# Kernel optimization log

Hardware: AMD Instinct MI355X
Metric: run time of the kernel (lower is better)

The kernel has to match this reference:

```python
import jax, jax.numpy as jnp
import numpy as np


def setup_inputs() -> dict:
    key = jax.random.key(0)
    k1, k2, k3, k4 = jax.random.split(key, 4)
    B, C, H, W = 8, 256, 64, 64
    x = jax.random.normal(k1, (B, C, H, W), dtype=jnp.float32)
    wq = jax.random.normal(k2, (1, C), dtype=jnp.float32) * (1.0 / np.sqrt(C))
    wk = jax.random.normal(k3, (1, C), dtype=jnp.float32) * (1.0 / np.sqrt(C))
    wv = jax.random.normal(k4, (C, C), dtype=jnp.float32) * (1.0 / np.sqrt(C))
    gamma = jnp.zeros((1,), dtype=jnp.float32)
    return {"x": x, "wq": wq, "wk": wk, "wv": wv, "gamma": gamma}


def reference(x, wq, wk, wv, gamma):
    B, C, H, W = x.shape
    N = H * W
    xf = x.reshape(B, C, N)                      # [B, C, N]
    # 1x1 convs == channel matmuls
    f = jnp.einsum('oc,bcn->bon', wq, xf)        # [B, 1, N]
    g = jnp.einsum('oc,bcn->bon', wk, xf)        # [B, 1, N]
    h = jnp.einsum('oc,bcn->bon', wv, xf)        # [B, C, N]
    # scores[b, i, j] = f[b, 0, i] * g[b, 0, j]  -> [B, N, N]
    scores = jnp.einsum('bi,bj->bij', f[:, 0, :], g[:, 0, :])
    # softmax over dim=1 (rows), matching torch F.softmax(..., dim=1)
    beta = jax.nn.softmax(scores, axis=1)        # [B, N, N]
    gam = gamma[0]
    o = (1.0 - gam) * jnp.einsum('bcn,bnm->bcm', h, beta) + gam * xf
    return o.reshape(B, C, H, W)
```

## Files before the change

### kernel.cpp

```cpp
#include <hip/hip_runtime.h>
#include <math.h>

#define BQ 8
#define CQ 256
#define NQ 4096
#define MT 128
#define NSUP 64

typedef short s16x8 __attribute__((ext_vector_type(8)));
typedef short s16x4 __attribute__((ext_vector_type(4)));
typedef float f32x4 __attribute__((ext_vector_type(4)));
typedef float f32x16 __attribute__((ext_vector_type(16)));
typedef unsigned int uint;

static __device__ __forceinline__ float4 ld4(const float* p) { return *(const float4*)p; }

static constexpr float LOG2E = 1.4426950408889634f;

static __device__ __forceinline__ short f2bf(float f) {
    return __builtin_bit_cast(short, (__bf16)f);
}
static __device__ __forceinline__ uint fkey(float f) {
    uint b = __builtin_bit_cast(uint, f);
    return b ^ (0x80000000u | (uint)((int)b >> 31));
}
static __device__ __forceinline__ float fdec(uint u) {
    uint b = (u & 0x80000000u) ? (u ^ 0x80000000u) : ~u;
    return __builtin_bit_cast(float, b);
}

__global__ void k_fg(const float* __restrict__ x, const float* __restrict__ wq,
                     const float* __restrict__ wk, float* __restrict__ fs,
                     float* __restrict__ g, short* __restrict__ xbf,
                     uint* __restrict__ fmxu, uint* __restrict__ fmnu) {
    int b = blockIdx.y;
    int t = threadIdx.x;
    int nl = (t & 31) * 2;
    int cg = t >> 5;
    int n = blockIdx.x * 64 + nl;
    const float* xb = x + (size_t)b * CQ * NQ + n;
    uint* xo = (uint*)(xbf + (size_t)b * CQ * NQ + n);
    float f0 = 0.f, f1 = 0.f, g0 = 0.f, g1 = 0.f;
    int c0 = cg * 32;
#pragma unroll 8
    for (int c = c0; c < c0 + 32; ++c) {
        float2 v = *(const float2*)&xb[(size_t)c * NQ];
        f0 = fmaf(wq[c], v.x, f0);
        f1 = fmaf(wq[c], v.y, f1);
        g0 = fmaf(wk[c], v.x, g0);
        g1 = fmaf(wk[c], v.y, g1);
        uint p = (uint)(unsigned short)f2bf(v.x) | ((uint)(unsigned short)f2bf(v.y) << 16);
        xo[c * (NQ / 2)] = p;
    }
    __shared__ float sf[8][64], sg2[8][64];
    sf[cg][nl] = f0;  sf[cg][nl + 1] = f1;
    sg2[cg][nl] = g0; sg2[cg][nl + 1] = g1;
    __syncthreads();
    if (t < 64) {
        float f = 0.f, gg = 0.f;
#pragma unroll
        for (int i = 0; i < 8; ++i) { f += sf[i][t]; gg += sg2[i][t]; }
        f *= LOG2E;
        fs[b * NQ + blockIdx.x * 64 + t] = f;
        g[b * NQ + blockIdx.x * 64 + t]  = gg;
        float mx = f, mn = f;
#pragma unroll
        for (int off = 32; off; off >>= 1) {
            mx = fmaxf(mx, __shfl_xor(mx, off));
            mn = fminf(mn, __shfl_xor(mn, off));
        }
        if (t == 0) {
            atomicMax(&fmxu[b], fkey(mx));
            atomicMin(&fmnu[b], fkey(mn));
        }
    }
}

#define FLDS_OFF 98304
#define ZBUF_OFF 131072
#define SMEM_BYTES 133120

#define GSRC(p) (const __attribute__((address_space(1))) void*)(p)
#define LDST(p) (__attribute__((address_space(3))) void*)(p)

__global__ void __launch_bounds__(512, 2) k_attn(
    const short* __restrict__ xbf, const float* __restrict__ fsp,
    const float* __restrict__ gp, const uint* __restrict__ fmxu,
    const uint* __restrict__ fmnu, const float* __restrict__ wv,
    const float* __restrict__ x, const float* __restrict__ gamma,
    float* __restrict__ out) {
    __shared__ __align__(16) char smem[SMEM_BYTES];

    int bid = blockIdx.x;
    int b = bid & 7;
    int mblk = bid >> 3;
    int m0 = mblk * MT;
    int tid = threadIdx.x;
    int l = tid & 63;
    int w = tid >> 6;
    int ws = w & 1;
    int wm = (w >> 1) & 1;
    int wc = w >> 2;
    int col = l & 31;
    int hi = l >> 5;
    int q = l >> 4;
    int cr = l & 15;

    const short* xb = xbf + (size_t)b * CQ * NQ;
    const float* fb = fsp + b * NQ;

    int dst = tid * 16;
    int srow0 = tid >> 2;
    int srow1 = srow0 + 128;
    const short* src0 = xb + (size_t)srow0 * NQ + ((tid & 3) ^ ((srow0 >> 1) & 3)) * 8;
    const short* src1 = xb + (size_t)srow1 * NQ + ((tid & 3) ^ ((srow1 >> 1) & 3)) * 8;

    __builtin_amdgcn_global_load_lds(GSRC(fb + tid * 4),
        LDST(smem + FLDS_OFF + dst), 16, 0, 0);
    __builtin_amdgcn_global_load_lds(GSRC(fb + tid * 4 + 2048),
        LDST(smem + FLDS_OFF + 8192 + dst), 16, 0, 0);
#pragma unroll
    for (int k = 0; k < 4; ++k) {
        __builtin_amdgcn_global_load_lds(GSRC(src0 + k * 32),
            LDST(smem + k * 16384 + dst), 16, 0, 0);
        __builtin_amdgcn_global_load_lds(GSRC(src1 + k * 32),
            LDST(smem + k * 16384 + 8192 + dst), 16, 0, 0);
    }

    float fmx = fdec(fmxu[b]), fmn = fdec(fmnu[b]);
    const float* gb = gp + b * NQ;
    float gj[2], nM[2], zac[2] = {0.f, 0.f};
#pragma unroll
    for (int mt = 0; mt < 2; ++mt) {
        float gv = gb[m0 + wm * 64 + mt * 32 + col];
        gj[mt] = gv;
        nM[mt] = -((gv >= 0.f) ? gv * fmx : gv * fmn);
    }

    int rowoff[4], rkey[4];
#pragma unroll
    for (int ct = 0; ct < 4; ++ct) {
        int row = wc * 128 + ct * 32 + col;
        rowoff[ct] = row * 64;
        rkey[ct] = ((row >> 1) & 3) * 16;
    }

    f32x16 acc[4][2];
#pragma unroll
    for (int ct = 0; ct < 4; ++ct)
#pragma unroll
        for (int mt = 0; mt < 2; ++mt)
#pragma unroll
            for (int r = 0; r < 16; ++r) acc[ct][mt][r] = 0.f;

    asm volatile("s_waitcnt vmcnt(8)" ::: "memory");
    __builtin_amdgcn_s_barrier();
    const float* fl0 = (const float*)(smem + FLDS_OFF);
    float4 fc[4];
    {
        int n0 = ws * 32;
        fc[0] = *(const float4*)(fl0 + n0 + 8 * hi);
        fc[1] = *(const float4*)(fl0 + n0 + 8 * hi + 4);
        fc[2] = *(const float4*)(fl0 + n0 + 16 + 8 * hi);
        fc[3] = *(const float4*)(fl0 + n0 + 16 + 8 * hi + 4);
    }

    int rs = 0;
    int ssl = 4;
    for (int p = 0; p < NSUP; ++p) {
        asm volatile("s_waitcnt vmcnt(4)" ::: "memory");
        __builtin_amdgcn_s_barrier();
        {
            int chA = (2 * p + 4) & 127;
            __builtin_amdgcn_global_load_lds(GSRC(src0 + chA * 32),
                LDST(smem + ssl * 16384 + dst), 16, 0, 0);
            __builtin_amdgcn_global_load_lds(GSRC(src1 + chA * 32),
                LDST(smem + ssl * 16384 + 8192 + dst), 16, 0, 0);
            __builtin_amdgcn_global_load_lds(GSRC(src0 + chA * 32 + 32),
                LDST(smem + (ssl + 1) * 16384 + dst), 16, 0, 0);
            __builtin_amdgcn_global_load_lds(GSRC(src1 + chA * 32 + 32),
                LDST(smem + (ssl + 1) * 16384 + 8192 + dst), 16, 0, 0);
        }
        s16x8 bv[2][2];
#pragma unroll
        for (int kt = 0; kt < 2; ++kt) {
            float fq[8] = {fc[kt*2].x, fc[kt*2].y, fc[kt*2].z, fc[kt*2].w,
                           fc[kt*2+1].x, fc[kt*2+1].y, fc[kt*2+1].z, fc[kt*2+1].w};
#pragma unroll
            for (int mt = 0; mt < 2; ++mt) {
                float z = zac[mt];
#pragma unroll
                for (int i = 0; i < 8; ++i) {
                    float e = __builtin_amdgcn_exp2f(fmaf(fq[i], gj[mt], nM[mt]));
                    z += e;
                    bv[mt][kt][i] = f2bf(e);
                }
                zac[mt] = z;
            }
        }
        {
            int nn = ((2 * p + 2 + ws) & 127) * 32;
            fc[0] = *(const float4*)(fl0 + nn + 8 * hi);
            fc[1] = *(const float4*)(fl0 + nn + 8 * hi + 4);
            fc[2] = *(const float4*)(fl0 + nn + 16 + 8 * hi);
            fc[3] = *(const float4*)(fl0 + nn + 16 + 8 * hi + 4);
        }
        const char* cbuf = smem + (rs + ws) * 16384;
#pragma unroll
        for (int kt = 0; kt < 2; ++kt) {
            int lslot = (kt * 2 + hi) * 16;
#pragma unroll
            for (int ct = 0; ct < 4; ++ct) {
                s16x8 av = *(const s16x8*)(cbuf + rowoff[ct] + (lslot ^ rkey[ct]));
                acc[ct][0] = __builtin_amdgcn_mfma_f32_32x32x16_bf16(av, bv[0][kt], acc[ct][0], 0, 0, 0);
                acc[ct][1] = __builtin_amdgcn_mfma_f32_32x32x16_bf16(av, bv[1][kt], acc[ct][1], 0, 0, 0);
            }
        }
        rs += 2;  if (rs >= 6) rs -= 6;
        ssl += 2; if (ssl >= 6) ssl -= 6;
    }
    __syncthreads();

    float zf[2];
#pragma unroll
    for (int mt = 0; mt < 2; ++mt) {
        float z = zac[mt];
        z += __shfl_xor(z, 32);
        zf[mt] = z;
    }
    {
        float* zb = (float*)(smem + ZBUF_OFF);
        if (l < 32) {
#pragma unroll
            for (int mt = 0; mt < 2; ++mt) zb[w * 64 + mt * 32 + l] = zf[mt];
        }
        int p8 = wc * 2 + wm;
        float* mrg = (float*)(smem + p8 * 32768);
        if (ws == 1) {
#pragma unroll
            for (int ct = 0; ct < 4; ++ct)
#pragma unroll
                for (int mt = 0; mt < 2; ++mt) {
                    int fi = ct * 2 + mt;
#pragma unroll
                    for (int j = 0; j < 4; ++j) {
                        f32x4 v = {acc[ct][mt][4*j], acc[ct][mt][4*j+1],
                                   acc[ct][mt][4*j+2], acc[ct][mt][4*j+3]};
                        *(f32x4*)(mrg + ((fi * 4 + j) * 64 + l) * 4) = v;
                    }
                }
        }
        __syncthreads();
        if (ws == 0) {
#pragma unroll
            for (int ct = 0; ct < 4; ++ct)
#pragma unroll
                for (int mt = 0; mt < 2; ++mt) {
                    int fi = ct * 2 + mt;
#pragma unroll
                    for (int j = 0; j < 4; ++j) {
                        f32x4 o = *(const f32x4*)(mrg + ((fi * 4 + j) * 64 + l) * 4);
#pragma unroll
                        for (int i = 0; i < 4; ++i) acc[ct][mt][4*j+i] += o[i];
                    }
                }
        }
#pragma unroll
        for (int mt = 0; mt < 2; ++mt) zf[mt] += zb[(w ^ 1) * 64 + mt * 32 + col];
        __syncthreads();
    }

    if (ws == 0) {
        float rzl[2] = {1.0f / zf[0], 1.0f / zf[1]};
#pragma unroll
        for (int ct = 0; ct < 4; ++ct)
#pragma unroll
            for (int mt = 0; mt < 2; ++mt) {
                int mloc = wm * 64 + mt * 32 + col;
                int key = (mloc & 7) << 4;
#pragma unroll
                for (int j = 0; j < 4; ++j) {
                    int cb = (wc * 256 + ct * 64 + 16 * j + 8 * hi) ^ key;
                    s16x4 v;
#pragma unroll
                    for (int i = 0; i < 4; ++i) v[i] = f2bf(acc[ct][mt][4*j+i] * rzl[mt]);
                    *(s16x4*)(smem + mloc * 512 + cb) = v;
                }
            }
    }
    __syncthreads();

    int co0 = w * 32;
    f32x4 acc2[2][8];
#pragma unroll
    for (int j2 = 0; j2 < 2; ++j2)
#pragma unroll
        for (int jm2 = 0; jm2 < 8; ++jm2) acc2[j2][jm2] = (f32x4){0.f, 0.f, 0.f, 0.f};

#pragma unroll 2
    for (int ks = 0; ks < 8; ++ks) {
        s16x8 a2[2];
#pragma unroll
        for (int j2 = 0; j2 < 2; ++j2) {
            const float* wr = wv + (size_t)(co0 + j2 * 16 + cr) * CQ + ks * 32 + q * 8;
            float4 wa = ld4(wr);
            float4 wb = ld4(wr + 4);
            a2[j2][0] = f2bf(wa.x); a2[j2][1] = f2bf(wa.y);
            a2[j2][2] = f2bf(wa.z); a2[j2][3] = f2bf(wa.w);
            a2[j2][4] = f2bf(wb.x); a2[j2][5] = f2bf(wb.y);
            a2[j2][6] = f2bf(wb.z); a2[j2][7] = f2bf(wb.w);
        }
#pragma unroll
        for (int jm2 = 0; jm2 < 8; ++jm2) {
            int mloc = jm2 * 16 + cr;
            s16x8 b2 = *(const s16x8*)(smem + mloc * 512 + ((ks * 64 + q * 16) ^ ((mloc & 7) << 4)));
#pragma unroll
            for (int j2 = 0; j2 < 2; ++j2)
                acc2[j2][jm2] = __builtin_amdgcn_mfma_f32_16x16x32_bf16(a2[j2], b2, acc2[j2][jm2], 0, 0, 0);
        }
    }

    float gam = gamma[0];
    float omg = 1.f - gam;
    if (gam != 0.f) {
#pragma unroll
        for (int j2 = 0; j2 < 2; ++j2)
#pragma unroll
            for (int jm2 = 0; jm2 < 8; ++jm2)
#pragma unroll
                for (int r = 0; r < 4; ++r) {
                    int c_out = co0 + j2 * 16 + q * 4 + r;
                    size_t idx = ((size_t)b * CQ + c_out) * NQ + m0 + jm2 * 16 + cr;
                    __builtin_nontemporal_store(
                        fmaf(gam, x[idx], acc2[j2][jm2][r] * omg), out + idx);
                }
    } else {
#pragma unroll
        for (int j2 = 0; j2 < 2; ++j2)
#pragma unroll
            for (int jm2 = 0; jm2 < 8; ++jm2)
#pragma unroll
                for (int r = 0; r < 4; ++r) {
                    int c_out = co0 + j2 * 16 + q * 4 + r;
                    size_t idx = ((size_t)b * CQ + c_out) * NQ + m0 + jm2 * 16 + cr;
                    __builtin_nontemporal_store(acc2[j2][jm2][r] * omg, out + idx);
                }
    }
}

extern "C" void kernel_launch(void* const* d_in, const int* in_sizes, int n_in,
                              void* d_out, int out_size, void* d_ws, size_t ws_size,
                              hipStream_t stream) {
    const float* x     = (const float*)d_in[0];
    const float* wq    = (const float*)d_in[1];
    const float* wk    = (const float*)d_in[2];
    const float* wv    = (const float*)d_in[3];
    const float* gamma = (const float*)d_in[4];
    float* out = (float*)d_out;

    float* ws  = (float*)d_ws;
    float* fs  = ws;
    float* g   = ws + BQ * NQ;
    uint* fmxu = (uint*)(ws + 2 * BQ * NQ);
    uint* fmnu = fmxu + 8;
    short* xbf = (short*)(ws + 2 * BQ * NQ + 64);

    hipMemsetAsync(fmxu, 0x00, 32, stream);
    hipMemsetAsync(fmnu, 0xFF, 32, stream);
    hipLaunchKernelGGL(k_fg, dim3(NQ / 64, BQ), dim3(256), 0, stream,
                       x, wq, wk, fs, g, xbf, fmxu, fmnu);
    hipLaunchKernelGGL(k_attn, dim3(BQ * (NQ / MT)), dim3(512), 0, stream,
                       xbf, fs, g, fmxu, fmnu, wv, x, gamma, out);
}
```

Measured before the change: 121.9 us.

## Software-pipeline exp computation ahead of MFMA and strengthen LDS swizzle

The exp2/bf16 conversion of attention weights for the next iteration is computed after issuing the current iteration's MFMAs, using a double-buffered register array. This lets transcendental VALU work overlap with matrix-core execution instead of serializing before it. Separately, the LDS XOR swizzle key now also mixes row bits 3-4, which is meant to reduce bank conflicts on the A-operand reads. The extra register buffer and unroll-by-2 raise register pressure at a 2-blocks-per-CU launch bound.

New measurement: 123.9 us. About the same (+1.6%).

```diff
diff --git a/kernel.cpp b/kernel.cpp
--- a/kernel.cpp
+++ b/kernel.cpp
@@ -83,6 +83,8 @@
 #define GSRC(p) (const __attribute__((address_space(1))) void*)(p)
 #define LDST(p) (__attribute__((address_space(3))) void*)(p)
 
+#define SWZKEY(row) ((((row) >> 1) & 3) ^ (((row) >> 3) & 3))
+
 __global__ void __launch_bounds__(512, 2) k_attn(
     const short* __restrict__ xbf, const float* __restrict__ fsp,
     const float* __restrict__ gp, const uint* __restrict__ fmxu,
@@ -112,8 +114,8 @@
     int dst = tid * 16;
     int srow0 = tid >> 2;
     int srow1 = srow0 + 128;
-    const short* src0 = xb + (size_t)srow0 * NQ + ((tid & 3) ^ ((srow0 >> 1) & 3)) * 8;
-    const short* src1 = xb + (size_t)srow1 * NQ + ((tid & 3) ^ ((srow1 >> 1) & 3)) * 8;
+    const short* src0 = xb + (size_t)srow0 * NQ + ((tid & 3) ^ SWZKEY(srow0)) * 8;
+    const short* src1 = xb + (size_t)srow1 * NQ + ((tid & 3) ^ SWZKEY(srow1)) * 8;
 
     __builtin_amdgcn_global_load_lds(GSRC(fb + tid * 4),
         LDST(smem + FLDS_OFF + dst), 16, 0, 0);
@@ -142,7 +144,7 @@
     for (int ct = 0; ct < 4; ++ct) {
         int row = wc * 128 + ct * 32 + col;
         rowoff[ct] = row * 64;
-        rkey[ct] = ((row >> 1) & 3) * 16;
+        rkey[ct] = SWZKEY(row) * 16;
     }
 
     f32x16 acc[4][2];
@@ -156,6 +158,8 @@
     asm volatile("s_waitcnt vmcnt(8)" ::: "memory");
     __builtin_amdgcn_s_barrier();
     const float* fl0 = (const float*)(smem + FLDS_OFF);
+
+    s16x8 bvb[2][2][2];
     float4 fc[4];
     {
         int n0 = ws * 32;
@@ -164,9 +168,33 @@
         fc[2] = *(const float4*)(fl0 + n0 + 16 + 8 * hi);
         fc[3] = *(const float4*)(fl0 + n0 + 16 + 8 * hi + 4);
     }
+#pragma unroll
+    for (int kt = 0; kt < 2; ++kt) {
+        float fq[8] = {fc[kt*2].x, fc[kt*2].y, fc[kt*2].z, fc[kt*2].w,
+                       fc[kt*2+1].x, fc[kt*2+1].y, fc[kt*2+1].z, fc[kt*2+1].w};
+#pragma unroll
+        for (int mt = 0; mt < 2; ++mt) {
+            float z = zac[mt];
+#pragma unroll
+            for (int i = 0; i < 8; ++i) {
+                float e = __builtin_amdgcn_exp2f(fmaf(fq[i], gj[mt], nM[mt]));
+                z += e;
+                bvb[0][mt][kt][i] = f2bf(e);
+            }
+            zac[mt] = z;
+        }
+    }
+    {
+        int nn = (2 + ws) * 32;
+        fc[0] = *(const float4*)(fl0 + nn + 8 * hi);
+        fc[1] = *(const float4*)(fl0 + nn + 8 * hi + 4);
+        fc[2] = *(const float4*)(fl0 + nn + 16 + 8 * hi);
+        fc[3] = *(const float4*)(fl0 + nn + 16 + 8 * hi + 4);
+    }
 
     int rs = 0;
     int ssl = 4;
+#pragma unroll 2
     for (int p = 0; p < NSUP; ++p) {
         asm volatile("s_waitcnt vmcnt(4)" ::: "memory");
         __builtin_amdgcn_s_barrier();
@@ -181,40 +209,39 @@
             __builtin_amdgcn_global_load_lds(GSRC(src1 + chA * 32 + 32),
                 LDST(smem + (ssl + 1) * 16384 + 8192 + dst), 16, 0, 0);
         }
-        s16x8 bv[2][2];
+        const char* cbuf = smem + (rs + ws) * 16384;
 #pragma unroll
         for (int kt = 0; kt < 2; ++kt) {
-            float fq[8] = {fc[kt*2].x, fc[kt*2].y, fc[kt*2].z, fc[kt*2].w,
-                           fc[kt*2+1].x, fc[kt*2+1].y, fc[kt*2+1].z, fc[kt*2+1].w};
-#pragma unroll
-            for (int mt = 0; mt < 2; ++mt) {
-                float z = zac[mt];
-#pragma unroll
-                for (int i = 0; i < 8; ++i) {
-                    float e = __builtin_amdgcn_exp2f(fmaf(fq[i], gj[mt], nM[mt]));
-                    z += e;
-                    bv[mt][kt][i] = f2bf(e);
-                }
-                zac[mt] = z;
+            int lslot = (kt * 2 + hi) * 16;
+#pragma unroll
+            for (int ct = 0; ct < 4; ++ct) {
+                s16x8 av = *(const s16x8*)(cbuf + rowoff[ct] + (lslot ^ rkey[ct]));
+                acc[ct][0] = __builtin_amdgcn_mfma_f32_32x32x16_bf16(av, bvb[p & 1][0][kt], acc[ct][0], 0, 0, 0);
+                acc[ct][1] = __builtin_amdgcn_mfma_f32_32x32x16_bf16(av, bvb[p & 1][1][kt], acc[ct][1], 0, 0, 0);
             }
         }
-        {
-            int nn = ((2 * p + 2 + ws) & 127) * 32;
+        if (p + 1 < NSUP) {
+#pragma unroll
+            for (int kt = 0; kt < 2; ++kt) {
+                float fq[8] = {fc[kt*2].x, fc[kt*2].y, fc[kt*2].z, fc[kt*2].w,
+                               fc[kt*2+1].x, fc[kt*2+1].y, fc[kt*2+1].z, fc[kt*2+1].w};
+#pragma unroll
+                for (int mt = 0; mt < 2; ++mt) {
+                    float z = zac[mt];
+#pragma unroll
+                    for (int i = 0; i < 8; ++i) {
+                        float e = __builtin_amdgcn_exp2f(fmaf(fq[i], gj[mt], nM[mt]));
+                        z += e;
+                        bvb[(p + 1) & 1][mt][kt][i] = f2bf(e);
+                    }
+                    zac[mt] = z;
+                }
+            }
+            int nn = ((2 * p + 4 + ws) & 127) * 32;
             fc[0] = *(const float4*)(fl0 + nn + 8 * hi);
             fc[1] = *(const float4*)(fl0 + nn + 8 * hi + 4);
             fc[2] = *(const float4*)(fl0 + nn + 16 + 8 * hi);
             fc[3] = *(const float4*)(fl0 + nn + 16 + 8 * hi + 4);
-        }
-        const char* cbuf = smem + (rs + ws) * 16384;
-#pragma unroll
-        for (int kt = 0; kt < 2; ++kt) {
-            int lslot = (kt * 2 + hi) * 16;
-#pragma unroll
-            for (int ct = 0; ct < 4; ++ct) {
-                s16x8 av = *(const s16x8*)(cbuf + rowoff[ct] + (lslot ^ rkey[ct]));
-                acc[ct][0] = __builtin_amdgcn_mfma_f32_32x32x16_bf16(av, bv[0][kt], acc[ct][0], 0, 0, 0);
-                acc[ct][1] = __builtin_amdgcn_mfma_f32_32x32x16_bf16(av, bv[1][kt], acc[ct][1], 0, 0, 0);
-            }
         }
         rs += 2;  if (rs >= 6) rs -= 6;
         ssl += 2; if (ssl >= 6) ssl -= 6;
```
